# Performance work log

Hardware: AMD Instinct MI355X
Metric: run time of the kernel (lower is better)

The kernel has to match this reference:

```python
import jax, jax.numpy as jnp
import numpy as np

EPS = 1e-9

def setup_inputs() -> dict:
    key = jax.random.key(0)
    k1, k2, k3, k4 = jax.random.split(key, 4)
    B, D, M, R, C = 1024, 16, 4, 4096, 64
    x = jax.random.normal(k1, (B, D), dtype=jnp.float32)
    centers = jax.random.normal(k2, (D, M), dtype=jnp.float32)
    widths = jnp.ones((D, M), dtype=jnp.float32)
    consequents = jax.random.normal(k3, (R, D + 1, C), dtype=jnp.float32)
    rules = jax.random.randint(k4, (R, D), 0, M)  # rule -> MF index per input dim
    return {"x": x, "centers": centers, "widths": widths,
            "consequents": consequents, "rules": rules}

def reference(x, centers, widths, consequents, rules):
    B, D = x.shape
    # Gaussian membership values: [B, D, M]
    mfs = jnp.exp(-(x[:, :, None] - centers[None]) ** 2 / (2.0 * widths[None] ** 2)) + EPS
    # Gather per-rule MFs: rule_mfs[b, d, r] = mfs[b, d, rules[r, d]] -> [B, D, R]
    rule_mfs = jnp.take_along_axis(mfs, rules.T[None, :, :], axis=2)
    # Product firing strengths and normalization: [B, R]
    fs = jnp.prod(rule_mfs, axis=1)
    nfs = fs / (fs.sum(axis=1, keepdims=True) + EPS)
    # Extended input with bias: [B, D+1]
    x_ext = jnp.concatenate([x, jnp.ones((B, 1), dtype=x.dtype)], axis=1)
    # NOTE: faithful to the original torch code: 'bi,rjc->brc' has no shared
    # contraction index, so it sums x_ext over i and consequents over j.
    rule_out = jnp.einsum('br,brc->bc', nfs,
                          jnp.einsum('bi,rjc->brc', x_ext, consequents))
    return rule_out, nfs, x_ext
```

## Files before the change

### kernel.cpp

```cpp
#include <hip/hip_runtime.h>
#include <hip/hip_bf16.h>

typedef __attribute__((ext_vector_type(8))) short short8;
typedef __attribute__((ext_vector_type(4))) short short4v;
typedef __attribute__((ext_vector_type(4))) float floatx4;
typedef __attribute__((ext_vector_type(4))) unsigned int uintx4;
typedef __attribute__((ext_vector_type(4))) int intx4;
typedef unsigned int u32;
typedef unsigned short u16;

#define NB 1024
#define ND 16
#define NM 4
#define NR 4096
#define NC 64
#define EPSF 1e-9f
#define KSPLIT 16

__device__ inline u16 f2bf(float f) {
    u32 u;
    __builtin_memcpy(&u, &f, 4);
    u32 lsb = (u >> 16) & 1;
    u += 0x7fffu + lsb;
    return (u16)(u >> 16);
}

__global__ __launch_bounds__(256) void k_pack(const int* __restrict__ rules,
                                              u32* __restrict__ packed) {
    int r = blockIdx.x * 256 + threadIdx.x;
    const int* q = rules + (size_t)r * ND;
    u32 pk = 0;
#pragma unroll
    for (int i = 0; i < 4; ++i) {
        intx4 v = *(const intx4*)(q + i * 4);
#pragma unroll
        for (int e = 0; e < 4; ++e) pk |= ((u32)(v[e] & 3)) << (2 * (i * 4 + e));
    }
    packed[r] = pk;
}

__global__ __launch_bounds__(256) void k_mid(const float* __restrict__ cons,
                                             const float* __restrict__ x,
                                             const float* __restrict__ centers,
                                             const float* __restrict__ widths,
                                             const u32* __restrict__ packed,
                                             u16* __restrict__ s_consT,
                                             float* __restrict__ out_nfs,
                                             float* __restrict__ out_xe,
                                             float* __restrict__ sx) {
    __shared__ u16 tile[16][68];
    __shared__ float xv[16];
    __shared__ float mftab[64];
    __shared__ float gtab[1024];
    __shared__ float wred[4];
    __shared__ float s_inv;
    int bid = blockIdx.x;
    int tid = threadIdx.x;
    if (bid < 256) {
        int rbase = bid * 16;
        int c = tid & 63;
        int rr = tid >> 6;
#pragma unroll
        for (int it = 0; it < 4; ++it, rr += 4) {
            const float* p = cons + (size_t)(rbase + rr) * (ND + 1) * NC + c;
            float s = 0.f;
#pragma unroll
            for (int j = 0; j < ND + 1; ++j) s += p[j * NC];
            tile[rr][c] = f2bf(s);
        }
        __syncthreads();
        int cc = tid >> 2;
        int r0 = (tid & 3) * 4;
        short4v v;
#pragma unroll
        for (int e = 0; e < 4; ++e) v[e] = (short)tile[r0 + e][cc];
        *(short4v*)(s_consT + (size_t)cc * NR + rbase + r0) = v;
        return;
    }
    int b = bid - 256;
    if (tid < 16) {
        float raw = x[b * 16 + tid];
        xv[tid] = raw;
        out_xe[b * 17 + tid] = raw;
    }
    if (tid == 16) out_xe[b * 17 + 16] = 1.0f;
    __syncthreads();
    if (tid < 64) {
        float diff = xv[tid >> 2] - centers[tid];
        float w = widths[tid];
        mftab[tid] = __expf(-diff * diff / (2.f * w * w)) + EPSF;
    }
    if (tid == 0) {
        float s = 1.f;
        for (int i = 0; i < 16; ++i) s += xv[i];
        sx[b] = s;
    }
    __syncthreads();
    for (int idx = tid; idx < 1024; idx += 256) {
        int g = idx >> 8, i = idx & 255;
        const float* mf = mftab + g * 16;
        gtab[idx] = mf[0 + (i & 3)] * mf[4 + ((i >> 2) & 3)] *
                    mf[8 + ((i >> 4) & 3)] * mf[12 + ((i >> 6) & 3)];
    }
    __syncthreads();
    floatx4 f[4];
    float lsum = 0.f;
#pragma unroll
    for (int it = 0; it < 4; ++it) {
        int r = it * 1024 + tid * 4;
        uintx4 p = *(const uintx4*)(packed + r);
#pragma unroll
        for (int e = 0; e < 4; ++e) {
            u32 pk = p[e];
            f[it][e] = gtab[pk & 255] * gtab[256 + ((pk >> 8) & 255)] *
                       gtab[512 + ((pk >> 16) & 255)] * gtab[768 + (pk >> 24)];
            lsum += f[it][e];
        }
    }
    for (int off = 32; off; off >>= 1) lsum += __shfl_down(lsum, off, 64);
    if ((tid & 63) == 0) wred[tid >> 6] = lsum;
    __syncthreads();
    if (tid == 0) s_inv = 1.f / (wred[0] + wred[1] + wred[2] + wred[3] + EPSF);
    __syncthreads();
    float inv = s_inv;
    float* on = out_nfs + (size_t)b * NR;
#pragma unroll
    for (int it = 0; it < 4; ++it) {
        int r = it * 1024 + tid * 4;
        floatx4 v;
#pragma unroll
        for (int e = 0; e < 4; ++e) v[e] = f[it][e] * inv;
        *(floatx4*)(on + r) = v;
    }
}

__global__ __launch_bounds__(256) void k_gemm(const float* __restrict__ nfs,
                                              const u16* __restrict__ s_consT,
                                              float* __restrict__ part) {
    int rt = blockIdx.x;
    int ks = blockIdx.y;
    int tid = threadIdx.x;
    int wid = tid >> 6, lane = tid & 63;
    int arow = rt * 64 + wid * 16 + (lane & 15);
    int kbase = ks * (NR / KSPLIT) + (lane >> 4) * 8;
    const float* aptr = nfs + (size_t)arow * NR + kbase;
    const u16* bptr = s_consT + (size_t)(lane & 15) * NR + kbase;
    floatx4 acc[4] = {};
#pragma unroll
    for (int t = 0; t < (NR / KSPLIT) / 32; ++t) {
        floatx4 alo = *(const floatx4*)(aptr + t * 32);
        floatx4 ahi = *(const floatx4*)(aptr + t * 32 + 4);
        short8 af;
#pragma unroll
        for (int e = 0; e < 4; ++e) {
            af[e] = (short)f2bf(alo[e]);
            af[e + 4] = (short)f2bf(ahi[e]);
        }
#pragma unroll
        for (int cb = 0; cb < 4; ++cb) {
            short8 bf = *(const short8*)(bptr + (size_t)cb * 16 * NR + t * 32);
            acc[cb] = __builtin_amdgcn_mfma_f32_16x16x32_bf16(af, bf, acc[cb], 0, 0, 0);
        }
    }
    float* po = part + (size_t)ks * (NB * NC);
    int row0 = rt * 64 + wid * 16 + (lane >> 4) * 4;
#pragma unroll
    for (int cb = 0; cb < 4; ++cb)
#pragma unroll
        for (int reg = 0; reg < 4; ++reg)
            po[(size_t)(row0 + reg) * NC + cb * 16 + (lane & 15)] = acc[cb][reg];
}

__global__ __launch_bounds__(256) void k_out(const float* __restrict__ part,
                                             const float* __restrict__ sx,
                                             float* __restrict__ out0) {
    int t = blockIdx.x * 256 + threadIdx.x;
    float a = 0.f;
#pragma unroll
    for (int ks = 0; ks < KSPLIT; ++ks) a += part[(size_t)ks * (NB * NC) + t];
    out0[t] = a * sx[t >> 6];
}

extern "C" void kernel_launch(void* const* d_in, const int* in_sizes, int n_in,
                              void* d_out, int out_size, void* d_ws, size_t ws_size,
                              hipStream_t stream) {
    const float* x = (const float*)d_in[0];
    const float* centers = (const float*)d_in[1];
    const float* widths = (const float*)d_in[2];
    const float* cons = (const float*)d_in[3];
    const int* rules = (const int*)d_in[4];

    float* out = (float*)d_out;
    float* out_rule = out;
    float* out_nfs = out + NB * NC;
    float* out_xe = out + NB * NC + NB * NR;

    char* ws = (char*)d_ws;
    u16* s_consT = (u16*)ws;
    u32* packed = (u32*)(ws + (512 << 10));
    float* sx = (float*)(ws + (512 << 10) + (16 << 10));
    float* part = (float*)(ws + (512 << 10) + (24 << 10));

    k_pack<<<NR / 256, 256, 0, stream>>>(rules, packed);
    k_mid<<<256 + NB, 256, 0, stream>>>(cons, x, centers, widths, packed,
                                        s_consT, out_nfs, out_xe, sx);
    k_gemm<<<dim3(16, KSPLIT), 256, 0, stream>>>(out_nfs, s_consT, part);
    k_out<<<(NB * NC) / 256, 256, 0, stream>>>(part, sx, out_rule);
}
```

Measured before the change: 31.98 us.

## Feed GEMM a bf16 copy of unnormalized firing strengths and bf16 partials

k_mid now also writes a bf16 copy of the unnormalized firing strengths. The normalization and the sum(x_ext) factor are folded into a per-row scale that k_out applies. The GEMM reads bf16 A directly, which halves A traffic and removes the per-element conversion, and KSPLIT doubles to 32 for more blocks. Split-K partials are stored as bf16, which halves partial traffic per split, but there are now twice as many splits and each partial is rounded, so accuracy drops. k_mid writes an extra 8MB buffer.

```diff
diff --git a/kernel.cpp b/kernel.cpp
--- a/kernel.cpp
+++ b/kernel.cpp
@@ -15,7 +15,7 @@
 #define NR 4096
 #define NC 64
 #define EPSF 1e-9f
-#define KSPLIT 16
+#define KSPLIT 32
 
 __device__ inline u16 f2bf(float f) {
     u32 u;
@@ -46,8 +46,9 @@
                                              const u32* __restrict__ packed,
                                              u16* __restrict__ s_consT,
                                              float* __restrict__ out_nfs,
+                                             u16* __restrict__ fs_bf,
                                              float* __restrict__ out_xe,
-                                             float* __restrict__ sx) {
+                                             float* __restrict__ rowscale) {
     __shared__ u16 tile[16][68];
     __shared__ float xv[16];
     __shared__ float mftab[64];
@@ -90,11 +91,6 @@
         float w = widths[tid];
         mftab[tid] = __expf(-diff * diff / (2.f * w * w)) + EPSF;
     }
-    if (tid == 0) {
-        float s = 1.f;
-        for (int i = 0; i < 16; ++i) s += xv[i];
-        sx[b] = s;
-    }
     __syncthreads();
     for (int idx = tid; idx < 1024; idx += 256) {
         int g = idx >> 8, i = idx & 255;
@@ -123,62 +119,71 @@
     if (tid == 0) s_inv = 1.f / (wred[0] + wred[1] + wred[2] + wred[3] + EPSF);
     __syncthreads();
     float inv = s_inv;
+    if (tid == 0) {
+        float s = 1.f;
+        for (int i = 0; i < 16; ++i) s += xv[i];
+        rowscale[b] = s * inv;
+    }
     float* on = out_nfs + (size_t)b * NR;
+    u16* ob = fs_bf + (size_t)b * NR;
 #pragma unroll
     for (int it = 0; it < 4; ++it) {
         int r = it * 1024 + tid * 4;
         floatx4 v;
-#pragma unroll
-        for (int e = 0; e < 4; ++e) v[e] = f[it][e] * inv;
+        short4v bv;
+#pragma unroll
+        for (int e = 0; e < 4; ++e) {
+            v[e] = f[it][e] * inv;
+            bv[e] = (short)f2bf(f[it][e]);
+        }
         *(floatx4*)(on + r) = v;
-    }
-}
-
-__global__ __launch_bounds__(256) void k_gemm(const float* __restrict__ nfs,
+        *(short4v*)(ob + r) = bv;
+    }
+}
+
+__global__ __launch_bounds__(256) void k_gemm(const u16* __restrict__ fs_bf,
                                               const u16* __restrict__ s_consT,
-                                              float* __restrict__ part) {
+                                              u16* __restrict__ part) {
     int rt = blockIdx.x;
     int ks = blockIdx.y;
     int tid = threadIdx.x;
     int wid = tid >> 6, lane = tid & 63;
     int arow = rt * 64 + wid * 16 + (lane & 15);
     int kbase = ks * (NR / KSPLIT) + (lane >> 4) * 8;
-    const float* aptr = nfs + (size_t)arow * NR + kbase;
+    const u16* aptr = fs_bf + (size_t)arow * NR + kbase;
     const u16* bptr = s_consT + (size_t)(lane & 15) * NR + kbase;
     floatx4 acc[4] = {};
 #pragma unroll
     for (int t = 0; t < (NR / KSPLIT) / 32; ++t) {
-        floatx4 alo = *(const floatx4*)(aptr + t * 32);
-        floatx4 ahi = *(const floatx4*)(aptr + t * 32 + 4);
-        short8 af;
-#pragma unroll
-        for (int e = 0; e < 4; ++e) {
-            af[e] = (short)f2bf(alo[e]);
-            af[e + 4] = (short)f2bf(ahi[e]);
-        }
+        short8 af = *(const short8*)(aptr + t * 32);
 #pragma unroll
         for (int cb = 0; cb < 4; ++cb) {
             short8 bf = *(const short8*)(bptr + (size_t)cb * 16 * NR + t * 32);
             acc[cb] = __builtin_amdgcn_mfma_f32_16x16x32_bf16(af, bf, acc[cb], 0, 0, 0);
         }
     }
-    float* po = part + (size_t)ks * (NB * NC);
+    u16* po = part + (size_t)ks * (NB * NC);
     int row0 = rt * 64 + wid * 16 + (lane >> 4) * 4;
 #pragma unroll
     for (int cb = 0; cb < 4; ++cb)
 #pragma unroll
         for (int reg = 0; reg < 4; ++reg)
-            po[(size_t)(row0 + reg) * NC + cb * 16 + (lane & 15)] = acc[cb][reg];
-}
-
-__global__ __launch_bounds__(256) void k_out(const float* __restrict__ part,
-                                             const float* __restrict__ sx,
+            po[(size_t)(row0 + reg) * NC + cb * 16 + (lane & 15)] = f2bf(acc[cb][reg]);
+}
+
+__global__ __launch_bounds__(256) void k_out(const u16* __restrict__ part,
+                                             const float* __restrict__ rowscale,
                                              float* __restrict__ out0) {
     int t = blockIdx.x * 256 + threadIdx.x;
     float a = 0.f;
 #pragma unroll
-    for (int ks = 0; ks < KSPLIT; ++ks) a += part[(size_t)ks * (NB * NC) + t];
-    out0[t] = a * sx[t >> 6];
+    for (int ks = 0; ks < KSPLIT; ++ks) {
+        u32 u = ((u32)part[(size_t)ks * (NB * NC) + t]) << 16;
+        float v;
+        __builtin_memcpy(&v, &u, 4);
+        a += v;
+    }
+    out0[t] = a * rowscale[t >> 6];
 }
 
 extern "C" void kernel_launch(void* const* d_in, const int* in_sizes, int n_in,
@@ -198,12 +203,13 @@
     char* ws = (char*)d_ws;
     u16* s_consT = (u16*)ws;
     u32* packed = (u32*)(ws + (512 << 10));
-    float* sx = (float*)(ws + (512 << 10) + (16 << 10));
-    float* part = (float*)(ws + (512 << 10) + (24 << 10));
+    float* rowscale = (float*)(ws + (512 << 10) + (16 << 10));
+    u16* fs_bf = (u16*)(ws + (512 << 10) + (24 << 10));
+    u16* part = (u16*)(ws + (512 << 10) + (24 << 10) + (size_t)NB * NR * 2);
 
     k_pack<<<NR / 256, 256, 0, stream>>>(rules, packed);
     k_mid<<<256 + NB, 256, 0, stream>>>(cons, x, centers, widths, packed,
-                                        s_consT, out_nfs, out_xe, sx);
-    k_gemm<<<dim3(16, KSPLIT), 256, 0, stream>>>(out_nfs, s_consT, part);
-    k_out<<<(NB * NC) / 256, 256, 0, stream>>>(part, sx, out_rule);
-}
+                                        s_consT, out_nfs, fs_bf, out_xe, rowscale);
+    k_gemm<<<dim3(16, KSPLIT), 256, 0, stream>>>(fs_bf, s_consT, part);
+    k_out<<<(NB * NC) / 256, 256, 0, stream>>>(part, rowscale, out_rule);
+}
```

Result: no change. 31.61 us (-1.1%).

## Fuse firing-strength computation with MFMA reduction per 4-row block, drop split-K

Applied to the files above, without the earlier changes.

Merges the rules-packing kernel into the consequent-prep kernel. It also fuses membership, firing-strength and normalisation with the bf16 MFMA contraction into a single kernel in which each block handles 4 batch rows. Unnormalised strengths are staged as bf16 in LDS and multiplied directly against the transposed consequents. The per-row scale (sum of x_ext divided by the firing-strength sum) is applied at the end. This removes the full re-read of the nfs matrix, the split-K partial buffer, and the final reduction kernel. In exchange, 12 of the 16 MFMA A rows are zero, every block streams the whole consequent matrix from L2, and the nfs output is now written from bf16-rounded values, which loses precision.

```diff
diff --git a/kernel.cpp b/kernel.cpp
--- a/kernel.cpp
+++ b/kernel.cpp
@@ -4,7 +4,6 @@
 typedef __attribute__((ext_vector_type(8))) short short8;
 typedef __attribute__((ext_vector_type(4))) short short4v;
 typedef __attribute__((ext_vector_type(4))) float floatx4;
-typedef __attribute__((ext_vector_type(4))) unsigned int uintx4;
 typedef __attribute__((ext_vector_type(4))) int intx4;
 typedef unsigned int u32;
 typedef unsigned short u16;
@@ -15,7 +14,7 @@
 #define NR 4096
 #define NC 64
 #define EPSF 1e-9f
-#define KSPLIT 16
+#define PADK 4112
 
 __device__ inline u16 f2bf(float f) {
     u32 u;
@@ -24,161 +23,142 @@
     u += 0x7fffu + lsb;
     return (u16)(u >> 16);
 }
-
-__global__ __launch_bounds__(256) void k_pack(const int* __restrict__ rules,
-                                              u32* __restrict__ packed) {
-    int r = blockIdx.x * 256 + threadIdx.x;
-    const int* q = rules + (size_t)r * ND;
-    u32 pk = 0;
-#pragma unroll
-    for (int i = 0; i < 4; ++i) {
-        intx4 v = *(const intx4*)(q + i * 4);
-#pragma unroll
-        for (int e = 0; e < 4; ++e) pk |= ((u32)(v[e] & 3)) << (2 * (i * 4 + e));
-    }
-    packed[r] = pk;
+__device__ inline float bf2f(u16 v) {
+    u32 u = ((u32)v) << 16;
+    float f;
+    __builtin_memcpy(&f, &u, 4);
+    return f;
 }
 
-__global__ __launch_bounds__(256) void k_mid(const float* __restrict__ cons,
-                                             const float* __restrict__ x,
-                                             const float* __restrict__ centers,
-                                             const float* __restrict__ widths,
-                                             const u32* __restrict__ packed,
-                                             u16* __restrict__ s_consT,
-                                             float* __restrict__ out_nfs,
-                                             float* __restrict__ out_xe,
-                                             float* __restrict__ sx) {
+__global__ __launch_bounds__(256) void k_prep(const float* __restrict__ cons,
+                                              const int* __restrict__ rules,
+                                              u16* __restrict__ s_consT,
+                                              u32* __restrict__ packed) {
     __shared__ u16 tile[16][68];
-    __shared__ float xv[16];
-    __shared__ float mftab[64];
-    __shared__ float gtab[1024];
-    __shared__ float wred[4];
-    __shared__ float s_inv;
     int bid = blockIdx.x;
     int tid = threadIdx.x;
-    if (bid < 256) {
-        int rbase = bid * 16;
-        int c = tid & 63;
-        int rr = tid >> 6;
+    if (bid >= 256) {
+        int r = (bid - 256) * 256 + tid;
+        const int* q = rules + (size_t)r * ND;
+        u32 pk = 0;
 #pragma unroll
-        for (int it = 0; it < 4; ++it, rr += 4) {
-            const float* p = cons + (size_t)(rbase + rr) * (ND + 1) * NC + c;
-            float s = 0.f;
+        for (int i = 0; i < 4; ++i) {
+            intx4 v = *(const intx4*)(q + i * 4);
 #pragma unroll
-            for (int j = 0; j < ND + 1; ++j) s += p[j * NC];
-            tile[rr][c] = f2bf(s);
+            for (int e = 0; e < 4; ++e) pk |= ((u32)(v[e] & 3)) << (2 * (i * 4 + e));
         }
-        __syncthreads();
-        int cc = tid >> 2;
-        int r0 = (tid & 3) * 4;
-        short4v v;
-#pragma unroll
-        for (int e = 0; e < 4; ++e) v[e] = (short)tile[r0 + e][cc];
-        *(short4v*)(s_consT + (size_t)cc * NR + rbase + r0) = v;
+        packed[r] = pk;
         return;
     }
-    int b = bid - 256;
-    if (tid < 16) {
-        float raw = x[b * 16 + tid];
-        xv[tid] = raw;
-        out_xe[b * 17 + tid] = raw;
-    }
-    if (tid == 16) out_xe[b * 17 + 16] = 1.0f;
-    __syncthreads();
-    if (tid < 64) {
-        float diff = xv[tid >> 2] - centers[tid];
-        float w = widths[tid];
-        mftab[tid] = __expf(-diff * diff / (2.f * w * w)) + EPSF;
-    }
-    if (tid == 0) {
-        float s = 1.f;
-        for (int i = 0; i < 16; ++i) s += xv[i];
-        sx[b] = s;
+    int rbase = bid * 16;
+    int c = tid & 63;
+    int rr = tid >> 6;
+#pragma unroll
+    for (int it = 0; it < 4; ++it, rr += 4) {
+        const float* p = cons + (size_t)(rbase + rr) * (ND + 1) * NC + c;
+        float s = 0.f;
+#pragma unroll
+        for (int j = 0; j < ND + 1; ++j) s += p[j * NC];
+        tile[rr][c] = f2bf(s);
     }
     __syncthreads();
-    for (int idx = tid; idx < 1024; idx += 256) {
-        int g = idx >> 8, i = idx & 255;
-        const float* mf = mftab + g * 16;
-        gtab[idx] = mf[0 + (i & 3)] * mf[4 + ((i >> 2) & 3)] *
-                    mf[8 + ((i >> 4) & 3)] * mf[12 + ((i >> 6) & 3)];
+    int cc = tid >> 2;
+    int r0 = (tid & 3) * 4;
+    short4v v;
+#pragma unroll
+    for (int e = 0; e < 4; ++e) v[e] = (short)tile[r0 + e][cc];
+    *(short4v*)(s_consT + (size_t)cc * NR + rbase + r0) = v;
+}
+
+__global__ __launch_bounds__(256) void k_fused(const float* __restrict__ x,
+                                               const float* __restrict__ centers,
+                                               const float* __restrict__ widths,
+                                               const u32* __restrict__ packed,
+                                               const u16* __restrict__ s_consT,
+                                               float* __restrict__ out_nfs,
+                                               float* __restrict__ out_xe,
+                                               float* __restrict__ out_rule) {
+    __shared__ __align__(16) u16 afrag[4][PADK];
+    __shared__ float gtab4[4][1024];
+    __shared__ float mftab[4][64];
+    __shared__ float xv[4][16];
+    __shared__ float rs[4];
+    int b0 = blockIdx.x * 4;
+    int tid = threadIdx.x;
+    int w = tid >> 6, lane = tid & 63;
+
+    if (tid < 64) xv[tid >> 4][tid & 15] = x[b0 * 16 + tid];
+    if (tid < 68) {
+        int bb = tid / 17, ii = tid % 17;
+        out_xe[(size_t)(b0 + bb) * 17 + ii] = (ii < 16) ? x[(b0 + bb) * 16 + ii] : 1.0f;
     }
     __syncthreads();
-    floatx4 f[4];
+    {
+        int bb = tid >> 6, dm = tid & 63;
+        float diff = xv[bb][dm >> 2] - centers[dm];
+        float wd = widths[dm];
+        mftab[bb][dm] = __expf(-diff * diff / (2.f * wd * wd)) + EPSF;
+    }
+    __syncthreads();
+#pragma unroll
+    for (int it = 0; it < 16; ++it) {
+        int idx = it * 256 + tid;
+        int bb = idx >> 10, rest = idx & 1023, g = rest >> 8, i = rest & 255;
+        const float* mf = &mftab[bb][g * 16];
+        gtab4[bb][g * 256 + i] = mf[i & 3] * mf[4 + ((i >> 2) & 3)] *
+                                 mf[8 + ((i >> 4) & 3)] * mf[12 + ((i >> 6) & 3)];
+    }
+    __syncthreads();
+    const float* gt = gtab4[w];
     float lsum = 0.f;
+#pragma unroll 4
+    for (int it = 0; it < 64; ++it) {
+        int r = it * 64 + lane;
+        u32 pk = packed[r];
+        float f = gt[pk & 255] * gt[256 + ((pk >> 8) & 255)] *
+                  gt[512 + ((pk >> 16) & 255)] * gt[768 + (pk >> 24)];
+        afrag[w][r] = f2bf(f);
+        lsum += f;
+    }
 #pragma unroll
-    for (int it = 0; it < 4; ++it) {
-        int r = it * 1024 + tid * 4;
-        uintx4 p = *(const uintx4*)(packed + r);
+    for (int off = 32; off; off >>= 1) lsum += __shfl_xor(lsum, off, 64);
+    float inv = 1.f / (lsum + EPSF);
+    if (lane == 0) {
+        float s = 1.f;
 #pragma unroll
-        for (int e = 0; e < 4; ++e) {
-            u32 pk = p[e];
-            f[it][e] = gtab[pk & 255] * gtab[256 + ((pk >> 8) & 255)] *
-                       gtab[512 + ((pk >> 16) & 255)] * gtab[768 + (pk >> 24)];
-            lsum += f[it][e];
-        }
+        for (int i = 0; i < 16; ++i) s += xv[w][i];
+        rs[w] = s * inv;
     }
-    for (int off = 32; off; off >>= 1) lsum += __shfl_down(lsum, off, 64);
-    if ((tid & 63) == 0) wred[tid >> 6] = lsum;
+    float* on = out_nfs + (size_t)(b0 + w) * NR;
+#pragma unroll
+    for (int it = 0; it < 16; ++it) {
+        int r = it * 256 + lane * 4;
+        short4v v4 = *(const short4v*)&afrag[w][r];
+        floatx4 o;
+#pragma unroll
+        for (int e = 0; e < 4; ++e) o[e] = bf2f((u16)v4[e]) * inv;
+        *(floatx4*)(on + r) = o;
+    }
     __syncthreads();
-    if (tid == 0) s_inv = 1.f / (wred[0] + wred[1] + wred[2] + wred[3] + EPSF);
-    __syncthreads();
-    float inv = s_inv;
-    float* on = out_nfs + (size_t)b * NR;
-#pragma unroll
-    for (int it = 0; it < 4; ++it) {
-        int r = it * 1024 + tid * 4;
-        floatx4 v;
-#pragma unroll
-        for (int e = 0; e < 4; ++e) v[e] = f[it][e] * inv;
-        *(floatx4*)(on + r) = v;
+    int col = w * 16 + (lane & 15);
+    int row = lane & 15;
+    int ks = lane >> 4;
+    const u16* bptr = s_consT + (size_t)col * NR + ks * 8;
+    const u16* aptr = &afrag[row < 4 ? row : 0][ks * 8];
+    bool arow_ok = row < 4;
+    floatx4 acc = {};
+#pragma unroll 4
+    for (int kt = 0; kt < NR / 32; ++kt) {
+        short8 bf = *(const short8*)(bptr + kt * 32);
+        short8 af = {};
+        if (arow_ok) af = *(const short8*)(aptr + kt * 32);
+        acc = __builtin_amdgcn_mfma_f32_16x16x32_bf16(af, bf, acc, 0, 0, 0);
     }
-}
-
-__global__ __launch_bounds__(256) void k_gemm(const float* __restrict__ nfs,
-                                              const u16* __restrict__ s_consT,
-                                              float* __restrict__ part) {
-    int rt = blockIdx.x;
-    int ks = blockIdx.y;
-    int tid = threadIdx.x;
-    int wid = tid >> 6, lane = tid & 63;
-    int arow = rt * 64 + wid * 16 + (lane & 15);
-    int kbase = ks * (NR / KSPLIT) + (lane >> 4) * 8;
-    const float* aptr = nfs + (size_t)arow * NR + kbase;
-    const u16* bptr = s_consT + (size_t)(lane & 15) * NR + kbase;
-    floatx4 acc[4] = {};
-#pragma unroll
-    for (int t = 0; t < (NR / KSPLIT) / 32; ++t) {
-        floatx4 alo = *(const floatx4*)(aptr + t * 32);
-        floatx4 ahi = *(const floatx4*)(aptr + t * 32 + 4);
-        short8 af;
-#pragma unroll
-        for (int e = 0; e < 4; ++e) {
-            af[e] = (short)f2bf(alo[e]);
-            af[e + 4] = (short)f2bf(ahi[e]);
-        }
-#pragma unroll
-        for (int cb = 0; cb < 4; ++cb) {
-            short8 bf = *(const short8*)(bptr + (size_t)cb * 16 * NR + t * 32);
-            acc[cb] = __builtin_amdgcn_mfma_f32_16x16x32_bf16(af, bf, acc[cb], 0, 0, 0);
-        }
-    }
-    float* po = part + (size_t)ks * (NB * NC);
-    int row0 = rt * 64 + wid * 16 + (lane >> 4) * 4;
-#pragma unroll
-    for (int cb = 0; cb < 4; ++cb)
+    if (lane < 16) {
 #pragma unroll
         for (int reg = 0; reg < 4; ++reg)
-            po[(size_t)(row0 + reg) * NC + cb * 16 + (lane & 15)] = acc[cb][reg];
-}
-
-__global__ __launch_bounds__(256) void k_out(const float* __restrict__ part,
-                                             const float* __restrict__ sx,
-                                             float* __restrict__ out0) {
-    int t = blockIdx.x * 256 + threadIdx.x;
-    float a = 0.f;
-#pragma unroll
-    for (int ks = 0; ks < KSPLIT; ++ks) a += part[(size_t)ks * (NB * NC) + t];
-    out0[t] = a * sx[t >> 6];
+            out_rule[(size_t)(b0 + reg) * NC + col] = acc[reg] * rs[reg];
+    }
 }
 
 extern "C" void kernel_launch(void* const* d_in, const int* in_sizes, int n_in,
@@ -198,12 +178,8 @@
     char* ws = (char*)d_ws;
     u16* s_consT = (u16*)ws;
     u32* packed = (u32*)(ws + (512 << 10));
-    float* sx = (float*)(ws + (512 << 10) + (16 << 10));
-    float* part = (float*)(ws + (512 << 10) + (24 << 10));
 
-    k_pack<<<NR / 256, 256, 0, stream>>>(rules, packed);
-    k_mid<<<256 + NB, 256, 0, stream>>>(cons, x, centers, widths, packed,
-                                        s_consT, out_nfs, out_xe, sx);
-    k_gemm<<<dim3(16, KSPLIT), 256, 0, stream>>>(out_nfs, s_consT, part);
-    k_out<<<(NB * NC) / 256, 256, 0, stream>>>(part, sx, out_rule);
+    k_prep<<<272, 256, 0, stream>>>(cons, rules, s_consT, packed);
+    k_fused<<<NB / 4, 256, 0, stream>>>(x, centers, widths, packed, s_consT,
+                                        out_nfs, out_xe, out_rule);
 }
```

New measurement: 44.40 us. +38.9%, slower.

## Restructure GEMM split-K with in-block K halves and register prefetch

Applied to the files above, without the earlier changes.

The GEMM now uses 32 row tiles of 32 rows and 8 K-splits instead of 16 tiles of 64 rows and 16 K-splits. Each block splits its K range across two wave pairs and sums the halves through shared memory, so the partial buffer that k_out reads is half as large. The inner loop also double-buffers the A and B register loads to hide global latency. The sx computation is moved later in k_mid. The trade-off is an extra __syncthreads and LDS round trip, plus more registers used for prefetching.

```diff
diff --git a/kernel.cpp b/kernel.cpp
--- a/kernel.cpp
+++ b/kernel.cpp
@@ -15,7 +15,7 @@
 #define NR 4096
 #define NC 64
 #define EPSF 1e-9f
-#define KSPLIT 16
+#define KS 8
 
 __device__ inline u16 f2bf(float f) {
     u32 u;
@@ -90,11 +90,6 @@
         float w = widths[tid];
         mftab[tid] = __expf(-diff * diff / (2.f * w * w)) + EPSF;
     }
-    if (tid == 0) {
-        float s = 1.f;
-        for (int i = 0; i < 16; ++i) s += xv[i];
-        sx[b] = s;
-    }
     __syncthreads();
     for (int idx = tid; idx < 1024; idx += 256) {
         int g = idx >> 8, i = idx & 255;
@@ -123,6 +118,11 @@
     if (tid == 0) s_inv = 1.f / (wred[0] + wred[1] + wred[2] + wred[3] + EPSF);
     __syncthreads();
     float inv = s_inv;
+    if (tid == 0) {
+        float s = 1.f;
+        for (int i = 0; i < 16; ++i) s += xv[i];
+        sx[b] = s;
+    }
     float* on = out_nfs + (size_t)b * NR;
 #pragma unroll
     for (int it = 0; it < 4; ++it) {
@@ -137,38 +137,67 @@
 __global__ __launch_bounds__(256) void k_gemm(const float* __restrict__ nfs,
                                               const u16* __restrict__ s_consT,
                                               float* __restrict__ part) {
+    __shared__ float red[2][16][64];
     int rt = blockIdx.x;
     int ks = blockIdx.y;
     int tid = threadIdx.x;
     int wid = tid >> 6, lane = tid & 63;
-    int arow = rt * 64 + wid * 16 + (lane & 15);
-    int kbase = ks * (NR / KSPLIT) + (lane >> 4) * 8;
-    const float* aptr = nfs + (size_t)arow * NR + kbase;
-    const u16* bptr = s_consT + (size_t)(lane & 15) * NR + kbase;
+    int rsub = wid & 1, khalf = wid >> 1;
+    int row = rt * 32 + rsub * 16 + (lane & 15);
+    int k0 = ks * 512 + khalf * 256 + (lane >> 4) * 8;
+    const float* aptr = nfs + (size_t)row * NR + k0;
+    const u16* bptr = s_consT + (size_t)(lane & 15) * NR + k0;
+
     floatx4 acc[4] = {};
-#pragma unroll
-    for (int t = 0; t < (NR / KSPLIT) / 32; ++t) {
-        floatx4 alo = *(const floatx4*)(aptr + t * 32);
-        floatx4 ahi = *(const floatx4*)(aptr + t * 32 + 4);
+    floatx4 a0 = *(const floatx4*)(aptr);
+    floatx4 a1 = *(const floatx4*)(aptr + 4);
+    short8 bv[4], bn[4];
+#pragma unroll
+    for (int cb = 0; cb < 4; ++cb) bv[cb] = *(const short8*)(bptr + (size_t)cb * 16 * NR);
+#pragma unroll
+    for (int t = 0; t < 8; ++t) {
+        floatx4 na0, na1;
+        if (t < 7) {
+            na0 = *(const floatx4*)(aptr + (t + 1) * 32);
+            na1 = *(const floatx4*)(aptr + (t + 1) * 32 + 4);
+#pragma unroll
+            for (int cb = 0; cb < 4; ++cb)
+                bn[cb] = *(const short8*)(bptr + (size_t)cb * 16 * NR + (t + 1) * 32);
+        }
         short8 af;
 #pragma unroll
         for (int e = 0; e < 4; ++e) {
-            af[e] = (short)f2bf(alo[e]);
-            af[e + 4] = (short)f2bf(ahi[e]);
-        }
-#pragma unroll
-        for (int cb = 0; cb < 4; ++cb) {
-            short8 bf = *(const short8*)(bptr + (size_t)cb * 16 * NR + t * 32);
-            acc[cb] = __builtin_amdgcn_mfma_f32_16x16x32_bf16(af, bf, acc[cb], 0, 0, 0);
-        }
-    }
-    float* po = part + (size_t)ks * (NB * NC);
-    int row0 = rt * 64 + wid * 16 + (lane >> 4) * 4;
-#pragma unroll
-    for (int cb = 0; cb < 4; ++cb)
-#pragma unroll
-        for (int reg = 0; reg < 4; ++reg)
-            po[(size_t)(row0 + reg) * NC + cb * 16 + (lane & 15)] = acc[cb][reg];
+            af[e] = (short)f2bf(a0[e]);
+            af[e + 4] = (short)f2bf(a1[e]);
+        }
+#pragma unroll
+        for (int cb = 0; cb < 4; ++cb)
+            acc[cb] = __builtin_amdgcn_mfma_f32_16x16x32_bf16(af, bv[cb], acc[cb], 0, 0, 0);
+        if (t < 7) {
+            a0 = na0; a1 = na1;
+#pragma unroll
+            for (int cb = 0; cb < 4; ++cb) bv[cb] = bn[cb];
+        }
+    }
+    int rloc = (lane >> 4) * 4;
+    if (khalf == 1) {
+#pragma unroll
+        for (int cb = 0; cb < 4; ++cb)
+#pragma unroll
+            for (int reg = 0; reg < 4; ++reg)
+                red[rsub][rloc + reg][cb * 16 + (lane & 15)] = acc[cb][reg];
+    }
+    __syncthreads();
+    if (khalf == 0) {
+        float* po = part + (size_t)ks * (NB * NC);
+#pragma unroll
+        for (int cb = 0; cb < 4; ++cb)
+#pragma unroll
+            for (int reg = 0; reg < 4; ++reg) {
+                float v = acc[cb][reg] + red[rsub][rloc + reg][cb * 16 + (lane & 15)];
+                po[(size_t)(rt * 32 + rsub * 16 + rloc + reg) * NC + cb * 16 + (lane & 15)] = v;
+            }
+    }
 }
 
 __global__ __launch_bounds__(256) void k_out(const float* __restrict__ part,
@@ -177,7 +206,7 @@
     int t = blockIdx.x * 256 + threadIdx.x;
     float a = 0.f;
 #pragma unroll
-    for (int ks = 0; ks < KSPLIT; ++ks) a += part[(size_t)ks * (NB * NC) + t];
+    for (int ks = 0; ks < KS; ++ks) a += part[(size_t)ks * (NB * NC) + t];
     out0[t] = a * sx[t >> 6];
 }
 
@@ -204,6 +233,6 @@
     k_pack<<<NR / 256, 256, 0, stream>>>(rules, packed);
     k_mid<<<256 + NB, 256, 0, stream>>>(cons, x, centers, widths, packed,
                                         s_consT, out_nfs, out_xe, sx);
-    k_gemm<<<dim3(16, KSPLIT), 256, 0, stream>>>(out_nfs, s_consT, part);
+    k_gemm<<<dim3(32, KS), 256, 0, stream>>>(out_nfs, s_consT, part);
     k_out<<<(NB * NC) / 256, 256, 0, stream>>>(part, sx, out_rule);
 }
```

Result: no change. 31.94 us (-0.1%).
